# Optimization experiments

Hardware: AMD Instinct MI355X
Metric: run time of the kernel (lower is better)

## Reference

```python
import jax, jax.numpy as jnp
import numpy as np

B, S, E, H = 4, 2048, 1024, 16
D = E // H  # head dim = 64


def setup_inputs() -> dict:
    key0 = jax.random.key(0)
    ks = jax.random.split(key0, 8)
    key = jax.random.normal(ks[0], (B, S, E), dtype=jnp.float32)
    query = jax.random.normal(ks[1], (B, S, E), dtype=jnp.float32)
    value = jax.random.normal(ks[2], (B, S, E), dtype=jnp.float32)
    # causal mask, broadcastable over heads: [B, 1, S, S]; avoids all-masked rows
    mask = jnp.broadcast_to(jnp.tril(jnp.ones((S, S), dtype=jnp.int32)), (B, 1, S, S))
    sc = 1.0 / np.sqrt(E)
    Wq = jax.random.normal(ks[3], (E, E), dtype=jnp.float32) * sc  # nn.Linear weight [out,in]
    Wk = jax.random.normal(ks[4], (E, E), dtype=jnp.float32) * sc
    Wv = jax.random.normal(ks[5], (E, E), dtype=jnp.float32) * sc
    Wo = jax.random.normal(ks[6], (E, E), dtype=jnp.float32) * sc
    bo = jax.random.normal(ks[7], (E,), dtype=jnp.float32) * 0.01
    return {"key": key, "query": query, "value": value, "mask": mask,
            "Wq": Wq, "Wk": Wk, "Wv": Wv, "Wo": Wo, "bo": bo}


def reference(key, query, value, mask, Wq, Wk, Wv, Wo, bo):
    b, s, _ = key.shape
    sq = query.shape[1]
    # projections (nn.Linear: x @ W^T)
    k = (key @ Wk.T).reshape(b, s, H, D).transpose(0, 2, 1, 3)     # [B,H,S,D]
    q = (query @ Wq.T).reshape(b, sq, H, D).transpose(0, 2, 1, 3)  # [B,H,Sq,D]
    v = (value @ Wv.T).reshape(b, s, H, D).transpose(0, 2, 1, 3)   # [B,H,S,D]
    scores = jnp.einsum('bhqd,bhkd->bhqk', q, k)                   # [B,H,Sq,S]
    # original masks BEFORE scaling (-inf survives the divide)
    scores = jnp.where(mask == 0, -jnp.inf, scores)
    scores = scores / jnp.sqrt(jnp.asarray(D, scores.dtype))
    attn = jax.nn.softmax(scores, axis=-1)
    val = jnp.einsum('bhqk,bhkd->bhqd', attn, v)                   # [B,H,Sq,D]
    val = val.transpose(0, 2, 1, 3).reshape(b, s, H * D)           # [B,S,E]
    return val @ Wo.T + bo
```

## Files before the change

kernel.cpp:

```cpp
#include <hip/hip_runtime.h>
#include <hip/hip_bf16.h>
#include <stdint.h>

#define Bk 4
#define Sk 2048
#define Ek 1024
#define Hk 16
#define Dk 64
#define Mk (Bk*Sk)

typedef __hip_bfloat16 bf16;
typedef __attribute__((ext_vector_type(8))) short bf16x8;
typedef __attribute__((ext_vector_type(4))) float f32x4;

__device__ __forceinline__ unsigned short f2bf(float f) {
    __hip_bfloat16 h = __float2bfloat16(f);
    return __builtin_bit_cast(unsigned short, h);
}

__device__ __forceinline__ void gld_lds16(const void* g, void* l) {
    __builtin_amdgcn_global_load_lds(
        (const __attribute__((address_space(1))) unsigned int*)g,
        (__attribute__((address_space(3))) unsigned int*)l, 16, 0, 0);
}

__global__ __launch_bounds__(256)
void conv_qkv(const float* __restrict__ q, const float* __restrict__ k,
              const float* __restrict__ v,
              ushort4* __restrict__ qb, ushort4* __restrict__ kb2,
              ushort4* __restrict__ vb)
{
    const int NQ = (Mk * Ek) / 4;
    int i = blockIdx.x * 256 + threadIdx.x;
    const int tot = 3 * NQ;
    for (; i < tot; i += gridDim.x * 256) {
        const float4* sp; ushort4* dp; int j;
        if (i < NQ)            { sp = (const float4*)q; dp = qb;  j = i; }
        else if (i < 2 * NQ)   { sp = (const float4*)k; dp = kb2; j = i - NQ; }
        else                   { sp = (const float4*)v; dp = vb;  j = i - 2 * NQ; }
        float4 x = sp[j];
        ushort4 o; o.x = f2bf(x.x); o.y = f2bf(x.y); o.z = f2bf(x.z); o.w = f2bf(x.w);
        dp[j] = o;
    }
}

__global__ __launch_bounds__(256)
void conv_w(const float* __restrict__ wq, const float* __restrict__ wk,
            const float* __restrict__ wv, const float* __restrict__ wo,
            ushort4* __restrict__ wqb, ushort4* __restrict__ wkb,
            ushort4* __restrict__ wvb, ushort4* __restrict__ wob)
{
    const int NW = (Ek * Ek) / 4;
    int i = blockIdx.x * 256 + threadIdx.x;
    const int tot = 4 * NW;
    for (; i < tot; i += gridDim.x * 256) {
        int rgn = i / NW, j = i - rgn * NW;
        const float4* sp = rgn == 0 ? (const float4*)wq :
                           rgn == 1 ? (const float4*)wk :
                           rgn == 2 ? (const float4*)wv : (const float4*)wo;
        ushort4* dp = rgn == 0 ? wqb : rgn == 1 ? wkb : rgn == 2 ? wvb : wob;
        float sc = (rgn == 0) ? 0.125f : 1.0f;
        float4 x = sp[j];
        ushort4 o; o.x = f2bf(x.x * sc); o.y = f2bf(x.y * sc);
        o.z = f2bf(x.z * sc); o.w = f2bf(x.w * sc);
        dp[j] = o;
    }
}

template<int EPI>
__global__ __launch_bounds__(256)
void gemm_bt(const bf16* __restrict__ A, const bf16* __restrict__ Bw,
             void* __restrict__ Cout, const float* __restrict__ bias)
{
    __shared__ bf16 As[128 * 64];
    __shared__ bf16 Bs[128 * 64];
    const int t = threadIdx.x, w = t >> 6, lane = t & 63;
    const int lo = lane & 15, hi = lane >> 4;
    const int wm = w >> 1, wn = w & 1;
    const int n0 = blockIdx.x * 128, m0 = blockIdx.y * 128;

    f32x4 acc[4][4] = {};

    const bf16* Ab = A  + (size_t)m0 * Ek;
    const bf16* Bb = Bw + (size_t)n0 * Ek;

    for (int kt = 0; kt < Ek; kt += 64) {
#pragma unroll
        for (int i = 0; i < 4; ++i) {
            int c = (w * 4 + i) * 64 + lane;
            int r = c >> 3, cb = c & 7, scb = cb ^ (r & 7);
            gld_lds16(Ab + (size_t)r * Ek + kt + scb * 8, &As[(w * 4 + i) * 512]);
            gld_lds16(Bb + (size_t)r * Ek + kt + scb * 8, &Bs[(w * 4 + i) * 512]);
        }
        __syncthreads();
#pragma unroll
        for (int kd = 0; kd < 2; ++kd) {
            bf16x8 av[4], bv[4];
#pragma unroll
            for (int mf = 0; mf < 4; ++mf) {
                int r = wm * 64 + mf * 16 + lo;
                int cb = (kd * 4 + hi) ^ (r & 7);
                av[mf] = *(const bf16x8*)&As[r * 64 + cb * 8];
            }
#pragma unroll
            for (int nf = 0; nf < 4; ++nf) {
                int r = wn * 64 + nf * 16 + lo;
                int cb = (kd * 4 + hi) ^ (r & 7);
                bv[nf] = *(const bf16x8*)&Bs[r * 64 + cb * 8];
            }
#pragma unroll
            for (int mf = 0; mf < 4; ++mf)
#pragma unroll
                for (int nf = 0; nf < 4; ++nf)
                    acc[mf][nf] = __builtin_amdgcn_mfma_f32_16x16x32_bf16(
                        av[mf], bv[nf], acc[mf][nf], 0, 0, 0);
        }
        __syncthreads();
    }
#pragma unroll
    for (int mf = 0; mf < 4; ++mf)
#pragma unroll
        for (int nf = 0; nf < 4; ++nf)
#pragma unroll
            for (int r = 0; r < 4; ++r) {
                int m = m0 + wm * 64 + mf * 16 + hi * 4 + r;
                int n = n0 + wn * 64 + nf * 16 + lo;
                float vv = acc[mf][nf][r];
                if constexpr (EPI == 0) {
                    ((bf16*)Cout)[(size_t)m * Ek + n] = __float2bfloat16(vv);
                } else if constexpr (EPI == 1) {
                    int b = m >> 11, s = m & (Sk - 1);
                    ((bf16*)Cout)[((size_t)(b * 1024 + n)) * Sk + s] = __float2bfloat16(vv);
                } else {
                    ((float*)Cout)[(size_t)m * Ek + n] = vv + bias[n];
                }
            }
}

__global__ __launch_bounds__(64)
void attn_fwd(const bf16* __restrict__ Qp, const bf16* __restrict__ Kp,
              const bf16* __restrict__ Vt, bf16* __restrict__ AO)
{
    __shared__ bf16 Pl[32 * 64];
    const int lane = threadIdx.x;
    const int lo = lane & 15, hi = lane >> 4;
    const int qt = blockIdx.x, h = blockIdx.y, b = blockIdx.z;
    const int q0 = qt * 32;

    bf16x8 qf[2][2];
#pragma unroll
    for (int mf = 0; mf < 2; ++mf)
#pragma unroll
        for (int kd = 0; kd < 2; ++kd)
            qf[mf][kd] = *(const bf16x8*)&Qp[(size_t)(b * Sk + q0 + mf * 16 + lo) * Ek
                                            + h * 64 + kd * 32 + hi * 8];

    f32x4 acc[2][4] = {};
    float mrow[2][4], lrow[2][4];
#pragma unroll
    for (int mf = 0; mf < 2; ++mf)
#pragma unroll
        for (int r = 0; r < 4; ++r) { mrow[mf][r] = -1e30f; lrow[mf][r] = 0.f; }

    for (int kb = 0; kb < q0 + 32; kb += 64) {
        f32x4 s[2][4] = {};
#pragma unroll
        for (int nf = 0; nf < 4; ++nf) {
            const bf16* kbase = &Kp[(size_t)(b * Sk + kb + nf * 16 + lo) * Ek + h * 64 + hi * 8];
            bf16x8 k0 = *(const bf16x8*)kbase;
            bf16x8 k1 = *(const bf16x8*)(kbase + 32);
#pragma unroll
            for (int mf = 0; mf < 2; ++mf) {
                s[mf][nf] = __builtin_amdgcn_mfma_f32_16x16x32_bf16(qf[mf][0], k0, s[mf][nf], 0, 0, 0);
                s[mf][nf] = __builtin_amdgcn_mfma_f32_16x16x32_bf16(qf[mf][1], k1, s[mf][nf], 0, 0, 0);
            }
        }
        if (kb + 64 > q0) {
#pragma unroll
            for (int mf = 0; mf < 2; ++mf)
#pragma unroll
                for (int nf = 0; nf < 4; ++nf)
#pragma unroll
                    for (int r = 0; r < 4; ++r) {
                        int q = q0 + mf * 16 + hi * 4 + r;
                        int key = kb + nf * 16 + lo;
                        if (key > q) s[mf][nf][r] = -1e30f;
                    }
        }
        float sf[2][4];
#pragma unroll
        for (int mf = 0; mf < 2; ++mf)
#pragma unroll
            for (int r = 0; r < 4; ++r) {
                float v = fmaxf(fmaxf(s[mf][0][r], s[mf][1][r]), fmaxf(s[mf][2][r], s[mf][3][r]));
                v = fmaxf(v, __shfl_xor(v, 1));
                v = fmaxf(v, __shfl_xor(v, 2));
                v = fmaxf(v, __shfl_xor(v, 4));
                v = fmaxf(v, __shfl_xor(v, 8));
                float mnew = fmaxf(mrow[mf][r], v);
                sf[mf][r] = __expf(mrow[mf][r] - mnew);
                mrow[mf][r] = mnew;
            }
#pragma unroll
        for (int mf = 0; mf < 2; ++mf)
#pragma unroll
            for (int nf = 0; nf < 4; ++nf)
#pragma unroll
                for (int r = 0; r < 4; ++r)
                    s[mf][nf][r] = __expf(s[mf][nf][r] - mrow[mf][r]);
#pragma unroll
        for (int mf = 0; mf < 2; ++mf)
#pragma unroll
            for (int r = 0; r < 4; ++r) {
                float rs = s[mf][0][r] + s[mf][1][r] + s[mf][2][r] + s[mf][3][r];
                rs += __shfl_xor(rs, 1);
                rs += __shfl_xor(rs, 2);
                rs += __shfl_xor(rs, 4);
                rs += __shfl_xor(rs, 8);
                lrow[mf][r] = lrow[mf][r] * sf[mf][r] + rs;
#pragma unroll
                for (int nd = 0; nd < 4; ++nd) acc[mf][nd][r] *= sf[mf][r];
            }
#pragma unroll
        for (int mf = 0; mf < 2; ++mf)
#pragma unroll
            for (int nf = 0; nf < 4; ++nf)
#pragma unroll
                for (int r = 0; r < 4; ++r) {
                    int q = mf * 16 + hi * 4 + r;
                    int key = nf * 16 + lo;
                    int idx = q * 64 + ((((key >> 3) ^ (q & 7)) << 3) | (key & 7));
                    Pl[idx] = __float2bfloat16(s[mf][nf][r]);
                }
#pragma unroll
        for (int ks = 0; ks < 2; ++ks) {
            bf16x8 pa[2];
#pragma unroll
            for (int mf = 0; mf < 2; ++mf) {
                int q = mf * 16 + lo;
                int cb = (ks * 4 + hi) ^ (q & 7);
                pa[mf] = *(const bf16x8*)&Pl[q * 64 + cb * 8];
            }
#pragma unroll
            for (int nd = 0; nd < 4; ++nd) {
                bf16x8 vf = *(const bf16x8*)&Vt[(size_t)(b * 1024 + h * 64 + nd * 16 + lo) * Sk
                                                + kb + ks * 32 + hi * 8];
#pragma unroll
                for (int mf = 0; mf < 2; ++mf)
                    acc[mf][nd] = __builtin_amdgcn_mfma_f32_16x16x32_bf16(pa[mf], vf, acc[mf][nd], 0, 0, 0);
            }
        }
    }
#pragma unroll
    for (int mf = 0; mf < 2; ++mf)
#pragma unroll
        for (int r = 0; r < 4; ++r) {
            float inv = 1.0f / lrow[mf][r];
            int q = q0 + mf * 16 + hi * 4 + r;
#pragma unroll
            for (int nd = 0; nd < 4; ++nd)
                AO[(size_t)(b * Sk + q) * Ek + h * 64 + nd * 16 + lo] =
                    __float2bfloat16(acc[mf][nd][r] * inv);
        }
}

extern "C" void kernel_launch(void* const* d_in, const int* in_sizes, int n_in,
                              void* d_out, int out_size, void* d_ws, size_t ws_size,
                              hipStream_t stream)
{
    (void)in_sizes; (void)n_in; (void)out_size; (void)ws_size;
    const float* key   = (const float*)d_in[0];
    const float* query = (const float*)d_in[1];
    const float* value = (const float*)d_in[2];
    const float* Wq = (const float*)d_in[4];
    const float* Wk = (const float*)d_in[5];
    const float* Wv = (const float*)d_in[6];
    const float* Wo = (const float*)d_in[7];
    const float* bo = (const float*)d_in[8];

    char* ws = (char*)d_ws;
    bf16* Vin = (bf16*)ws; ws += (size_t)Mk * Ek * 2;
    bf16* Wqb = (bf16*)ws; ws += (size_t)Ek * Ek * 2;
    bf16* Wkb = (bf16*)ws; ws += (size_t)Ek * Ek * 2;
    bf16* Wvb = (bf16*)ws; ws += (size_t)Ek * Ek * 2;
    bf16* Wob = (bf16*)ws; ws += (size_t)Ek * Ek * 2;
    bf16* Qp  = (bf16*)ws; ws += (size_t)Mk * Ek * 2;
    bf16* Kp  = (bf16*)ws; ws += (size_t)Mk * Ek * 2;
    bf16* Vt  = (bf16*)ws; ws += (size_t)Mk * Ek * 2;
    bf16* AO  = (bf16*)ws; ws += (size_t)Mk * Ek * 2;

    bf16* Qin = (bf16*)d_out;
    bf16* Kin = Qin + (size_t)Mk * Ek;

    conv_qkv<<<4096, 256, 0, stream>>>(query, key, value,
                                       (ushort4*)Qin, (ushort4*)Kin, (ushort4*)Vin);
    conv_w<<<2048, 256, 0, stream>>>(Wq, Wk, Wv, Wo,
                                     (ushort4*)Wqb, (ushort4*)Wkb, (ushort4*)Wvb, (ushort4*)Wob);

    dim3 gg(Ek / 128, Mk / 128);
    gemm_bt<0><<<gg, 256, 0, stream>>>(Qin, Wqb, Qp, nullptr);
    gemm_bt<0><<<gg, 256, 0, stream>>>(Kin, Wkb, Kp, nullptr);
    gemm_bt<1><<<gg, 256, 0, stream>>>(Vin, Wvb, Vt, nullptr);

    attn_fwd<<<dim3(Sk / 32, Hk, Bk), 64, 0, stream>>>(Qp, Kp, Vt, AO);

    gemm_bt<2><<<gg, 256, 0, stream>>>(AO, Wob, d_out, bo);
}
```

Before: 500.8 us.

## Share K/V tiles across four waves via double-buffered LDS in attention

The attention kernel now runs four waves per block over a 128-query chunk. K and V tiles are staged into swizzled, double-buffered LDS with async global-to-LDS loads, so all waves share them instead of each wave loading from global memory. Query chunks are launched in reverse order so the longest causal rows start first. The cost is a block-wide barrier every tile, and waves with short causal ranges sit idle while others finish.

Result: no change. 501.4 us (+0.1%).

```diff
diff --git a/kernel.cpp b/kernel.cpp
--- a/kernel.cpp
+++ b/kernel.cpp
@@ -137,15 +137,26 @@
             }
 }
 
-__global__ __launch_bounds__(64)
-void attn_fwd(const bf16* __restrict__ Qp, const bf16* __restrict__ Kp,
-              const bf16* __restrict__ Vt, bf16* __restrict__ AO)
-{
-    __shared__ bf16 Pl[32 * 64];
-    const int lane = threadIdx.x;
+#define QCH 128
+#define KVB 64
+__global__ __launch_bounds__(256)
+void attn_fwd4(const bf16* __restrict__ Qp, const bf16* __restrict__ Kp,
+               const bf16* __restrict__ Vt, bf16* __restrict__ AO)
+{
+    __shared__ bf16 Kl[2][KVB * 64];
+    __shared__ bf16 Vl[2][64 * KVB];
+    __shared__ bf16 Pl[4][32 * 64];
+    const int t = threadIdx.x, w = t >> 6, lane = t & 63;
     const int lo = lane & 15, hi = lane >> 4;
-    const int qt = blockIdx.x, h = blockIdx.y, b = blockIdx.z;
-    const int q0 = qt * 32;
+    const int qc = (int)gridDim.x - 1 - (int)blockIdx.x;
+    const int h = blockIdx.y, b = blockIdx.z;
+    const int qbase = qc * QCH;
+    const int q0 = qbase + w * 32;
+    const int qe = q0 + 32;
+    const int ntiles = (qbase + QCH) / KVB;
+
+    const bf16* Kg = Kp + (size_t)(b * Sk) * Ek + h * 64;
+    const bf16* Vg = Vt + (size_t)(b * 1024 + h * 64) * Sk;
 
     bf16x8 qf[2][2];
 #pragma unroll
@@ -162,94 +173,120 @@
 #pragma unroll
         for (int r = 0; r < 4; ++r) { mrow[mf][r] = -1e30f; lrow[mf][r] = 0.f; }
 
-    for (int kb = 0; kb < q0 + 32; kb += 64) {
-        f32x4 s[2][4] = {};
-#pragma unroll
-        for (int nf = 0; nf < 4; ++nf) {
-            const bf16* kbase = &Kp[(size_t)(b * Sk + kb + nf * 16 + lo) * Ek + h * 64 + hi * 8];
-            bf16x8 k0 = *(const bf16x8*)kbase;
-            bf16x8 k1 = *(const bf16x8*)(kbase + 32);
-#pragma unroll
-            for (int mf = 0; mf < 2; ++mf) {
-                s[mf][nf] = __builtin_amdgcn_mfma_f32_16x16x32_bf16(qf[mf][0], k0, s[mf][nf], 0, 0, 0);
-                s[mf][nf] = __builtin_amdgcn_mfma_f32_16x16x32_bf16(qf[mf][1], k1, s[mf][nf], 0, 0, 0);
-            }
-        }
-        if (kb + 64 > q0) {
+#pragma unroll
+    for (int i = 0; i < 2; ++i) {
+        int c = w * 128 + i * 64 + lane;
+        int r = c >> 3, cb = c & 7, scb = cb ^ (r & 7);
+        gld_lds16(Kg + (size_t)r * Ek + scb * 8, &Kl[0][(w * 128 + i * 64) * 8]);
+        gld_lds16(Vg + (size_t)r * Sk + scb * 8, &Vl[0][(w * 128 + i * 64) * 8]);
+    }
+    __syncthreads();
+
+    for (int kt = 0; kt < ntiles; ++kt) {
+        const int kb = kt * KVB;
+        const int cur = kt & 1;
+        if (kt + 1 < ntiles) {
+            const int kb2 = kb + KVB;
+#pragma unroll
+            for (int i = 0; i < 2; ++i) {
+                int c = w * 128 + i * 64 + lane;
+                int r = c >> 3, cb = c & 7, scb = cb ^ (r & 7);
+                gld_lds16(Kg + (size_t)(kb2 + r) * Ek + scb * 8,
+                          &Kl[cur ^ 1][(w * 128 + i * 64) * 8]);
+                gld_lds16(Vg + (size_t)r * Sk + kb2 + scb * 8,
+                          &Vl[cur ^ 1][(w * 128 + i * 64) * 8]);
+            }
+        }
+        if (kb < qe) {
+            f32x4 s[2][4] = {};
+#pragma unroll
+            for (int nf = 0; nf < 4; ++nf) {
+                int rk = nf * 16 + lo;
+                bf16x8 k0 = *(const bf16x8*)&Kl[cur][rk * 64 + ((0 + hi) ^ (rk & 7)) * 8];
+                bf16x8 k1 = *(const bf16x8*)&Kl[cur][rk * 64 + ((4 + hi) ^ (rk & 7)) * 8];
+#pragma unroll
+                for (int mf = 0; mf < 2; ++mf) {
+                    s[mf][nf] = __builtin_amdgcn_mfma_f32_16x16x32_bf16(qf[mf][0], k0, s[mf][nf], 0, 0, 0);
+                    s[mf][nf] = __builtin_amdgcn_mfma_f32_16x16x32_bf16(qf[mf][1], k1, s[mf][nf], 0, 0, 0);
+                }
+            }
+            if (kb + KVB > q0) {
+#pragma unroll
+                for (int mf = 0; mf < 2; ++mf)
+#pragma unroll
+                    for (int nf = 0; nf < 4; ++nf)
+#pragma unroll
+                        for (int r = 0; r < 4; ++r) {
+                            int q = q0 + mf * 16 + hi * 4 + r;
+                            int key = kb + nf * 16 + lo;
+                            if (key > q) s[mf][nf][r] = -1e30f;
+                        }
+            }
+            float sf[2][4];
 #pragma unroll
             for (int mf = 0; mf < 2; ++mf)
 #pragma unroll
+                for (int r = 0; r < 4; ++r) {
+                    float v = fmaxf(fmaxf(s[mf][0][r], s[mf][1][r]), fmaxf(s[mf][2][r], s[mf][3][r]));
+                    v = fmaxf(v, __shfl_xor(v, 1));
+                    v = fmaxf(v, __shfl_xor(v, 2));
+                    v = fmaxf(v, __shfl_xor(v, 4));
+                    v = fmaxf(v, __shfl_xor(v, 8));
+                    float mnew = fmaxf(mrow[mf][r], v);
+                    sf[mf][r] = __expf(mrow[mf][r] - mnew);
+                    mrow[mf][r] = mnew;
+                }
+#pragma unroll
+            for (int mf = 0; mf < 2; ++mf)
+#pragma unroll
                 for (int nf = 0; nf < 4; ++nf)
 #pragma unroll
+                    for (int r = 0; r < 4; ++r)
+                        s[mf][nf][r] = __expf(s[mf][nf][r] - mrow[mf][r]);
+#pragma unroll
+            for (int mf = 0; mf < 2; ++mf)
+#pragma unroll
+                for (int r = 0; r < 4; ++r) {
+                    float rs = s[mf][0][r] + s[mf][1][r] + s[mf][2][r] + s[mf][3][r];
+                    rs += __shfl_xor(rs, 1);
+                    rs += __shfl_xor(rs, 2);
+                    rs += __shfl_xor(rs, 4);
+                    rs += __shfl_xor(rs, 8);
+                    lrow[mf][r] = lrow[mf][r] * sf[mf][r] + rs;
+#pragma unroll
+                    for (int nd = 0; nd < 4; ++nd) acc[mf][nd][r] *= sf[mf][r];
+                }
+#pragma unroll
+            for (int mf = 0; mf < 2; ++mf)
+#pragma unroll
+                for (int nf = 0; nf < 4; ++nf)
+#pragma unroll
                     for (int r = 0; r < 4; ++r) {
-                        int q = q0 + mf * 16 + hi * 4 + r;
-                        int key = kb + nf * 16 + lo;
-                        if (key > q) s[mf][nf][r] = -1e30f;
+                        int q = mf * 16 + hi * 4 + r;
+                        int key = nf * 16 + lo;
+                        int idx = q * 64 + ((((key >> 3) ^ (q & 7)) << 3) | (key & 7));
+                        Pl[w][idx] = __float2bfloat16(s[mf][nf][r]);
                     }
-        }
-        float sf[2][4];
-#pragma unroll
-        for (int mf = 0; mf < 2; ++mf)
-#pragma unroll
-            for (int r = 0; r < 4; ++r) {
-                float v = fmaxf(fmaxf(s[mf][0][r], s[mf][1][r]), fmaxf(s[mf][2][r], s[mf][3][r]));
-                v = fmaxf(v, __shfl_xor(v, 1));
-                v = fmaxf(v, __shfl_xor(v, 2));
-                v = fmaxf(v, __shfl_xor(v, 4));
-                v = fmaxf(v, __shfl_xor(v, 8));
-                float mnew = fmaxf(mrow[mf][r], v);
-                sf[mf][r] = __expf(mrow[mf][r] - mnew);
-                mrow[mf][r] = mnew;
-            }
-#pragma unroll
-        for (int mf = 0; mf < 2; ++mf)
-#pragma unroll
-            for (int nf = 0; nf < 4; ++nf)
-#pragma unroll
-                for (int r = 0; r < 4; ++r)
-                    s[mf][nf][r] = __expf(s[mf][nf][r] - mrow[mf][r]);
-#pragma unroll
-        for (int mf = 0; mf < 2; ++mf)
-#pragma unroll
-            for (int r = 0; r < 4; ++r) {
-                float rs = s[mf][0][r] + s[mf][1][r] + s[mf][2][r] + s[mf][3][r];
-                rs += __shfl_xor(rs, 1);
-                rs += __shfl_xor(rs, 2);
-                rs += __shfl_xor(rs, 4);
-                rs += __shfl_xor(rs, 8);
-                lrow[mf][r] = lrow[mf][r] * sf[mf][r] + rs;
-#pragma unroll
-                for (int nd = 0; nd < 4; ++nd) acc[mf][nd][r] *= sf[mf][r];
-            }
-#pragma unroll
-        for (int mf = 0; mf < 2; ++mf)
-#pragma unroll
-            for (int nf = 0; nf < 4; ++nf)
-#pragma unroll
-                for (int r = 0; r < 4; ++r) {
-                    int q = mf * 16 + hi * 4 + r;
-                    int key = nf * 16 + lo;
-                    int idx = q * 64 + ((((key >> 3) ^ (q & 7)) << 3) | (key & 7));
-                    Pl[idx] = __float2bfloat16(s[mf][nf][r]);
-                }
-#pragma unroll
-        for (int ks = 0; ks < 2; ++ks) {
-            bf16x8 pa[2];
-#pragma unroll
-            for (int mf = 0; mf < 2; ++mf) {
-                int q = mf * 16 + lo;
-                int cb = (ks * 4 + hi) ^ (q & 7);
-                pa[mf] = *(const bf16x8*)&Pl[q * 64 + cb * 8];
-            }
-#pragma unroll
-            for (int nd = 0; nd < 4; ++nd) {
-                bf16x8 vf = *(const bf16x8*)&Vt[(size_t)(b * 1024 + h * 64 + nd * 16 + lo) * Sk
-                                                + kb + ks * 32 + hi * 8];
-#pragma unroll
-                for (int mf = 0; mf < 2; ++mf)
-                    acc[mf][nd] = __builtin_amdgcn_mfma_f32_16x16x32_bf16(pa[mf], vf, acc[mf][nd], 0, 0, 0);
-            }
-        }
+#pragma unroll
+            for (int ks = 0; ks < 2; ++ks) {
+                bf16x8 pa[2];
+#pragma unroll
+                for (int mf = 0; mf < 2; ++mf) {
+                    int q = mf * 16 + lo;
+                    int cb = (ks * 4 + hi) ^ (q & 7);
+                    pa[mf] = *(const bf16x8*)&Pl[w][q * 64 + cb * 8];
+                }
+#pragma unroll
+                for (int nd = 0; nd < 4; ++nd) {
+                    int rv = nd * 16 + lo;
+                    bf16x8 vf = *(const bf16x8*)&Vl[cur][rv * 64 + ((ks * 4 + hi) ^ (rv & 7)) * 8];
+#pragma unroll
+                    for (int mf = 0; mf < 2; ++mf)
+                        acc[mf][nd] = __builtin_amdgcn_mfma_f32_16x16x32_bf16(pa[mf], vf, acc[mf][nd], 0, 0, 0);
+                }
+            }
+        }
+        __syncthreads();
     }
 #pragma unroll
     for (int mf = 0; mf < 2; ++mf)
@@ -302,7 +339,7 @@
     gemm_bt<0><<<gg, 256, 0, stream>>>(Kin, Wkb, Kp, nullptr);
     gemm_bt<1><<<gg, 256, 0, stream>>>(Vin, Wvb, Vt, nullptr);
 
-    attn_fwd<<<dim3(Sk / 32, Hk, Bk), 64, 0, stream>>>(Qp, Kp, Vt, AO);
+    attn_fwd4<<<dim3(Sk / QCH, Hk, Bk), 256, 0, stream>>>(Qp, Kp, Vt, AO);
 
     gemm_bt<2><<<gg, 256, 0, stream>>>(AO, Wob, d_out, bo);
 }
```

## Restructure attention with transposed scores, exp2 softmax, lazy rescale, reversed tile order

Applied to the files above, without the earlier changes.

The attention kernel now computes S^T (K as the A operand), so each lane holds one query row and the row max and sum need only two cross-lane shuffles. Q is prescaled by log2(e) in the weight conversion so the kernel can use exp2f. Rescaling of the accumulator is skipped unless the row max grows by more than 8. K and V fragments are prefetched at the top of each tile, P is written to LDS in packed 64-bit stores, MFMA sections are raised with setprio, and query tiles are launched in reverse order so the longest causal blocks start first. The lazy-rescale threshold lets unnormalized exponentials grow up to 2^8, which adds a small precision risk.

Result: faster. 488.6 us (-2.4%).

```diff
diff --git a/kernel.cpp b/kernel.cpp
--- a/kernel.cpp
+++ b/kernel.cpp
@@ -8,6 +8,7 @@
 #define Hk 16
 #define Dk 64
 #define Mk (Bk*Sk)
+#define KVB 64
 
 typedef __hip_bfloat16 bf16;
 typedef __attribute__((ext_vector_type(8))) short bf16x8;
@@ -16,6 +17,9 @@
 __device__ __forceinline__ unsigned short f2bf(float f) {
     __hip_bfloat16 h = __float2bfloat16(f);
     return __builtin_bit_cast(unsigned short, h);
+}
+__device__ __forceinline__ unsigned pack2bf(float a, float b) {
+    return (unsigned)f2bf(a) | ((unsigned)f2bf(b) << 16);
 }
 
 __device__ __forceinline__ void gld_lds16(const void* g, void* l) {
@@ -59,7 +63,7 @@
                            rgn == 1 ? (const float4*)wk :
                            rgn == 2 ? (const float4*)wv : (const float4*)wo;
         ushort4* dp = rgn == 0 ? wqb : rgn == 1 ? wkb : rgn == 2 ? wvb : wob;
-        float sc = (rgn == 0) ? 0.125f : 1.0f;
+        float sc = (rgn == 0) ? 0.125f * 1.44269504088896f : 1.0f;
         float4 x = sp[j];
         ushort4 o; o.x = f2bf(x.x * sc); o.y = f2bf(x.y * sc);
         o.z = f2bf(x.z * sc); o.w = f2bf(x.w * sc);
@@ -138,129 +142,152 @@
 }
 
 __global__ __launch_bounds__(64)
-void attn_fwd(const bf16* __restrict__ Qp, const bf16* __restrict__ Kp,
-              const bf16* __restrict__ Vt, bf16* __restrict__ AO)
+void attn_fwd1(const bf16* __restrict__ Qp, const bf16* __restrict__ Kp,
+               const bf16* __restrict__ Vt, bf16* __restrict__ AO)
 {
     __shared__ bf16 Pl[32 * 64];
     const int lane = threadIdx.x;
     const int lo = lane & 15, hi = lane >> 4;
-    const int qt = blockIdx.x, h = blockIdx.y, b = blockIdx.z;
+    const int qt = (int)gridDim.x - 1 - (int)blockIdx.x;
+    const int h = blockIdx.y, b = blockIdx.z;
     const int q0 = qt * 32;
+    const int ntiles = q0 / KVB + 1;
+
+    const bf16* Qg = Qp + (size_t)(b * Sk) * Ek + h * 64;
+    const bf16* Kg = Kp + (size_t)(b * Sk) * Ek + h * 64;
+    const bf16* Vg = Vt + (size_t)(b * 1024 + h * 64) * Sk;
 
     bf16x8 qf[2][2];
 #pragma unroll
     for (int mf = 0; mf < 2; ++mf)
 #pragma unroll
-        for (int kd = 0; kd < 2; ++kd)
-            qf[mf][kd] = *(const bf16x8*)&Qp[(size_t)(b * Sk + q0 + mf * 16 + lo) * Ek
-                                            + h * 64 + kd * 32 + hi * 8];
+        for (int sl = 0; sl < 2; ++sl)
+            qf[mf][sl] = *(const bf16x8*)&Qg[(size_t)(q0 + mf * 16 + lo) * Ek + sl * 32 + hi * 8];
 
     f32x4 acc[2][4] = {};
-    float mrow[2][4], lrow[2][4];
+    float mrow[2] = { -1e30f, -1e30f };
+    float lrow[2] = { 0.f, 0.f };
+
+    for (int kt = 0; kt < ntiles; ++kt) {
+        const int kb = kt * KVB;
+        bf16x8 kfr[4][2], vfr[4][2];
+#pragma unroll
+        for (int i = 0; i < 4; ++i) {
+            const bf16* kr = &Kg[(size_t)(kb + i * 16 + lo) * Ek + hi * 8];
+            kfr[i][0] = *(const bf16x8*)kr;
+            kfr[i][1] = *(const bf16x8*)(kr + 32);
+            const bf16* vr = &Vg[(size_t)(i * 16 + lo) * Sk + kb + hi * 8];
+            vfr[i][0] = *(const bf16x8*)vr;
+            vfr[i][1] = *(const bf16x8*)(vr + 32);
+        }
+        f32x4 sT[4][2] = {};
+        __builtin_amdgcn_s_setprio(1);
+#pragma unroll
+        for (int kf = 0; kf < 4; ++kf)
+#pragma unroll
+            for (int mf = 0; mf < 2; ++mf) {
+                sT[kf][mf] = __builtin_amdgcn_mfma_f32_16x16x32_bf16(kfr[kf][0], qf[mf][0], sT[kf][mf], 0, 0, 0);
+                sT[kf][mf] = __builtin_amdgcn_mfma_f32_16x16x32_bf16(kfr[kf][1], qf[mf][1], sT[kf][mf], 0, 0, 0);
+            }
+        __builtin_amdgcn_s_setprio(0);
+        if (kb + KVB > q0) {
+#pragma unroll
+            for (int kf = 0; kf < 4; ++kf)
+#pragma unroll
+                for (int mf = 0; mf < 2; ++mf)
+#pragma unroll
+                    for (int r = 0; r < 4; ++r)
+                        if (kb + kf * 16 + hi * 4 + r > q0 + mf * 16 + lo)
+                            sT[kf][mf][r] = -1e30f;
+        }
+        float pmax[2];
+#pragma unroll
+        for (int mf = 0; mf < 2; ++mf) {
+            float v0 = fmaxf(fmaxf(sT[0][mf][0], sT[0][mf][1]), fmaxf(sT[0][mf][2], sT[0][mf][3]));
+            float v1 = fmaxf(fmaxf(sT[1][mf][0], sT[1][mf][1]), fmaxf(sT[1][mf][2], sT[1][mf][3]));
+            float v2 = fmaxf(fmaxf(sT[2][mf][0], sT[2][mf][1]), fmaxf(sT[2][mf][2], sT[2][mf][3]));
+            float v3 = fmaxf(fmaxf(sT[3][mf][0], sT[3][mf][1]), fmaxf(sT[3][mf][2], sT[3][mf][3]));
+            float v = fmaxf(fmaxf(v0, v1), fmaxf(v2, v3));
+            v = fmaxf(v, __shfl_xor(v, 16));
+            v = fmaxf(v, __shfl_xor(v, 32));
+            pmax[mf] = v;
+        }
+        bool need = (pmax[0] > mrow[0] + 8.f) || (pmax[1] > mrow[1] + 8.f);
+        if (__any(need)) {
+            float sf[2];
+#pragma unroll
+            for (int mf = 0; mf < 2; ++mf) {
+                float mn = fmaxf(mrow[mf], pmax[mf]);
+                sf[mf] = exp2f(mrow[mf] - mn);
+                mrow[mf] = mn;
+                lrow[mf] *= sf[mf];
+            }
+#pragma unroll
+            for (int r = 0; r < 4; ++r) {
+                float a0 = __shfl(sf[0], hi * 4 + r);
+                float a1 = __shfl(sf[1], hi * 4 + r);
+#pragma unroll
+                for (int nd = 0; nd < 4; ++nd) { acc[0][nd][r] *= a0; acc[1][nd][r] *= a1; }
+            }
+        }
+        float rs[2] = { 0.f, 0.f };
+#pragma unroll
+        for (int kf = 0; kf < 4; ++kf)
+#pragma unroll
+            for (int mf = 0; mf < 2; ++mf)
+#pragma unroll
+                for (int r = 0; r < 4; ++r) {
+                    float p = exp2f(sT[kf][mf][r] - mrow[mf]);
+                    sT[kf][mf][r] = p;
+                    rs[mf] += p;
+                }
+#pragma unroll
+        for (int mf = 0; mf < 2; ++mf) {
+            float v = rs[mf];
+            v += __shfl_xor(v, 16);
+            v += __shfl_xor(v, 32);
+            lrow[mf] += v;
+        }
+#pragma unroll
+        for (int mf = 0; mf < 2; ++mf)
+#pragma unroll
+            for (int kf = 0; kf < 4; ++kf) {
+                int q = mf * 16 + lo;
+                int chunk = kf * 2 + (hi >> 1);
+                int idx = q * 64 + ((chunk ^ (q & 7)) * 8) + 4 * (hi & 1);
+                uint2 u;
+                u.x = pack2bf(sT[kf][mf][0], sT[kf][mf][1]);
+                u.y = pack2bf(sT[kf][mf][2], sT[kf][mf][3]);
+                *(uint2*)&Pl[idx] = u;
+            }
+        bf16x8 pa[2][2];
+#pragma unroll
+        for (int mf = 0; mf < 2; ++mf)
+#pragma unroll
+            for (int ks = 0; ks < 2; ++ks) {
+                int q = mf * 16 + lo;
+                pa[mf][ks] = *(const bf16x8*)&Pl[q * 64 + (((ks * 4 + hi) ^ (q & 7)) * 8)];
+            }
+        __builtin_amdgcn_s_setprio(1);
+#pragma unroll
+        for (int mf = 0; mf < 2; ++mf)
+#pragma unroll
+            for (int nd = 0; nd < 4; ++nd) {
+                acc[mf][nd] = __builtin_amdgcn_mfma_f32_16x16x32_bf16(pa[mf][0], vfr[nd][0], acc[mf][nd], 0, 0, 0);
+                acc[mf][nd] = __builtin_amdgcn_mfma_f32_16x16x32_bf16(pa[mf][1], vfr[nd][1], acc[mf][nd], 0, 0, 0);
+            }
+        __builtin_amdgcn_s_setprio(0);
+    }
 #pragma unroll
     for (int mf = 0; mf < 2; ++mf)
 #pragma unroll
-        for (int r = 0; r < 4; ++r) { mrow[mf][r] = -1e30f; lrow[mf][r] = 0.f; }
-
-    for (int kb = 0; kb < q0 + 32; kb += 64) {
-        f32x4 s[2][4] = {};
-#pragma unroll
-        for (int nf = 0; nf < 4; ++nf) {
-            const bf16* kbase = &Kp[(size_t)(b * Sk + kb + nf * 16 + lo) * Ek + h * 64 + hi * 8];
-            bf16x8 k0 = *(const bf16x8*)kbase;
-            bf16x8 k1 = *(const bf16x8*)(kbase + 32);
-#pragma unroll
-            for (int mf = 0; mf < 2; ++mf) {
-                s[mf][nf] = __builtin_amdgcn_mfma_f32_16x16x32_bf16(qf[mf][0], k0, s[mf][nf], 0, 0, 0);
-                s[mf][nf] = __builtin_amdgcn_mfma_f32_16x16x32_bf16(qf[mf][1], k1, s[mf][nf], 0, 0, 0);
-            }
-        }
-        if (kb + 64 > q0) {
-#pragma unroll
-            for (int mf = 0; mf < 2; ++mf)
-#pragma unroll
-                for (int nf = 0; nf < 4; ++nf)
-#pragma unroll
-                    for (int r = 0; r < 4; ++r) {
-                        int q = q0 + mf * 16 + hi * 4 + r;
-                        int key = kb + nf * 16 + lo;
-                        if (key > q) s[mf][nf][r] = -1e30f;
-                    }
-        }
-        float sf[2][4];
-#pragma unroll
-        for (int mf = 0; mf < 2; ++mf)
-#pragma unroll
-            for (int r = 0; r < 4; ++r) {
-                float v = fmaxf(fmaxf(s[mf][0][r], s[mf][1][r]), fmaxf(s[mf][2][r], s[mf][3][r]));
-                v = fmaxf(v, __shfl_xor(v, 1));
-                v = fmaxf(v, __shfl_xor(v, 2));
-                v = fmaxf(v, __shfl_xor(v, 4));
-                v = fmaxf(v, __shfl_xor(v, 8));
-                float mnew = fmaxf(mrow[mf][r], v);
-                sf[mf][r] = __expf(mrow[mf][r] - mnew);
-                mrow[mf][r] = mnew;
-            }
-#pragma unroll
-        for (int mf = 0; mf < 2; ++mf)
-#pragma unroll
-            for (int nf = 0; nf < 4; ++nf)
-#pragma unroll
-                for (int r = 0; r < 4; ++r)
-                    s[mf][nf][r] = __expf(s[mf][nf][r] - mrow[mf][r]);
-#pragma unroll
-        for (int mf = 0; mf < 2; ++mf)
-#pragma unroll
-            for (int r = 0; r < 4; ++r) {
-                float rs = s[mf][0][r] + s[mf][1][r] + s[mf][2][r] + s[mf][3][r];
-                rs += __shfl_xor(rs, 1);
-                rs += __shfl_xor(rs, 2);
-                rs += __shfl_xor(rs, 4);
-                rs += __shfl_xor(rs, 8);
-                lrow[mf][r] = lrow[mf][r] * sf[mf][r] + rs;
-#pragma unroll
-                for (int nd = 0; nd < 4; ++nd) acc[mf][nd][r] *= sf[mf][r];
-            }
-#pragma unroll
-        for (int mf = 0; mf < 2; ++mf)
-#pragma unroll
-            for (int nf = 0; nf < 4; ++nf)
-#pragma unroll
-                for (int r = 0; r < 4; ++r) {
-                    int q = mf * 16 + hi * 4 + r;
-                    int key = nf * 16 + lo;
-                    int idx = q * 64 + ((((key >> 3) ^ (q & 7)) << 3) | (key & 7));
-                    Pl[idx] = __float2bfloat16(s[mf][nf][r]);
-                }
-#pragma unroll
-        for (int ks = 0; ks < 2; ++ks) {
-            bf16x8 pa[2];
-#pragma unroll
-            for (int mf = 0; mf < 2; ++mf) {
-                int q = mf * 16 + lo;
-                int cb = (ks * 4 + hi) ^ (q & 7);
-                pa[mf] = *(const bf16x8*)&Pl[q * 64 + cb * 8];
-            }
-#pragma unroll
-            for (int nd = 0; nd < 4; ++nd) {
-                bf16x8 vf = *(const bf16x8*)&Vt[(size_t)(b * 1024 + h * 64 + nd * 16 + lo) * Sk
-                                                + kb + ks * 32 + hi * 8];
-#pragma unroll
-                for (int mf = 0; mf < 2; ++mf)
-                    acc[mf][nd] = __builtin_amdgcn_mfma_f32_16x16x32_bf16(pa[mf], vf, acc[mf][nd], 0, 0, 0);
-            }
-        }
-    }
-#pragma unroll
-    for (int mf = 0; mf < 2; ++mf)
-#pragma unroll
         for (int r = 0; r < 4; ++r) {
-            float inv = 1.0f / lrow[mf][r];
+            float il = 1.0f / __shfl(lrow[mf], hi * 4 + r);
             int q = q0 + mf * 16 + hi * 4 + r;
 #pragma unroll
             for (int nd = 0; nd < 4; ++nd)
                 AO[(size_t)(b * Sk + q) * Ek + h * 64 + nd * 16 + lo] =
-                    __float2bfloat16(acc[mf][nd][r] * inv);
+                    __float2bfloat16(acc[mf][nd][r] * il);
         }
 }
 
@@ -302,7 +329,7 @@
     gemm_bt<0><<<gg, 256, 0, stream>>>(Kin, Wkb, Kp, nullptr);
     gemm_bt<1><<<gg, 256, 0, stream>>>(Vin, Wvb, Vt, nullptr);
 
-    attn_fwd<<<dim3(Sk / 32, Hk, Bk), 64, 0, stream>>>(Qp, Kp, Vt, AO);
+    attn_fwd1<<<dim3(Sk / 32, Hk, Bk), 64, 0, stream>>>(Qp, Kp, Vt, AO);
 
     gemm_bt<2><<<gg, 256, 0, stream>>>(AO, Wob, d_out, bo);
 }
```
